# Kernel optimization log

Measured on AMD Instinct MI355X. Metric: run time of the kernel, lower is better.

Reference implementation:

```python
import jax, jax.numpy as jnp
import numpy as np

B, DIM, N = 4, 256, 2048
HEADS, DIM_HEAD = 8, 64
HIDDEN = HEADS * DIM_HEAD
SCALE = DIM_HEAD ** -0.5


def setup_inputs() -> dict:
    key = jax.random.key(0)
    k0, k1, k2, k3 = jax.random.split(key, 4)
    x = jax.random.normal(k0, (B, DIM, N), dtype=jnp.float32)
    # Conv1d kernel-size-1 weights == plain matrices over channels
    w_qkv = jax.random.normal(k1, (3 * HIDDEN, DIM), dtype=jnp.float32) * (DIM ** -0.5)
    w_out = jax.random.normal(k2, (DIM, HIDDEN), dtype=jnp.float32) * (HIDDEN ** -0.5)
    b_out = jax.random.normal(k3, (DIM,), dtype=jnp.float32) * 0.01
    return {"x": x, "w_qkv": w_qkv, "w_out": w_out, "b_out": b_out}


def reference(x, w_qkv, w_out, b_out):
    b, c, n = x.shape
    # 1x1 conv projection: [3H, C] x [b, C, n] -> [b, 3H, n]
    qkv = jnp.einsum('oc,bcn->bon', w_qkv, x)
    q, k, v = jnp.split(qkv, 3, axis=1)
    # [b, heads, dim_head, n]
    q = q.reshape(b, HEADS, DIM_HEAD, n) * SCALE
    k = k.reshape(b, HEADS, DIM_HEAD, n)
    v = v.reshape(b, HEADS, DIM_HEAD, n)
    sim = jnp.einsum('bhcn,bhcm->bhnm', q, k)          # [b,h,n,n]
    attn = jax.nn.softmax(sim, axis=-1)
    out = jnp.einsum('bhnm,bhcm->bhcn', attn, v)       # [b,h,dh,n]
    out = out.reshape(b, HIDDEN, n)
    return jnp.einsum('oc,bcn->bon', w_out, out) + b_out[None, :, None]
```

## Files before the change

### kernel.cpp

```cpp
#include <hip/hip_runtime.h>
#include <math.h>

#define BB 4
#define CDIM 256
#define NN 2048
#define HEADS 8
#define DH 64
#define HIDDEN 512
#define THREEH 1536
#define QSCALE 0.18033688011112042f

typedef __attribute__((ext_vector_type(8))) short bf16x8;
typedef __attribute__((ext_vector_type(4))) float f32x4;

static __device__ inline unsigned short f2bf(float f) {
    unsigned u = __float_as_uint(f);
    u += 0x7fff + ((u >> 16) & 1);
    return (unsigned short)(u >> 16);
}
#if __has_builtin(__builtin_amdgcn_cvt_pk_bf16_f32)
static __device__ inline unsigned pk2(float a, float b) {
    auto v = __builtin_amdgcn_cvt_pk_bf16_f32(a, b);
    return __builtin_bit_cast(unsigned, v);
}
#else
static __device__ inline unsigned pk2(float a, float b) {
    return (unsigned)f2bf(a) | ((unsigned)f2bf(b) << 16);
}
#endif
#if __has_builtin(__builtin_amdgcn_exp2f)
#define EXP2(x) __builtin_amdgcn_exp2f(x)
#else
#define EXP2(x) exp2f(x)
#endif
#define MFMA16(a, b, c) __builtin_amdgcn_mfma_f32_16x16x32_bf16(a, b, c, 0, 0, 0)
#define SWZC(row, ch) ((((ch) ^ ((row) & 7)) << 3))

__global__ __launch_bounds__(256) void prep_all(const float* __restrict__ x,
                                                const float* __restrict__ wqkv,
                                                const float* __restrict__ wout,
                                                unsigned short* __restrict__ Xt,
                                                unsigned* __restrict__ Wqb,
                                                unsigned* __restrict__ Wob) {
    __shared__ float Ls[64][65];
    const int bx = blockIdx.x;
    if (bx < 512) {
        const int n0 = (bx & 31) * 64, c0 = ((bx >> 5) & 3) * 64, b = bx >> 7;
        const int t = threadIdx.x;
        const int r16 = t >> 4, c16 = t & 15;
#pragma unroll
        for (int s = 0; s < 4; ++s) {
            const int c = s * 16 + r16;
            float4 v = *(const float4*)&x[((size_t)(b * CDIM + c0 + c)) * NN + n0 + c16 * 4];
            *(float4*)&Ls[c][c16 * 4] = v;
        }
        __syncthreads();
#pragma unroll
        for (int s = 0; s < 4; ++s) {
            const int n = s * 16 + r16;
            const int c4 = c16 * 4;
            uint2 u;
            u.x = pk2(Ls[c4][n], Ls[c4 + 1][n]);
            u.y = pk2(Ls[c4 + 2][n], Ls[c4 + 3][n]);
            *(uint2*)&Xt[((size_t)(b * NN) + n0 + n) * CDIM + c0 + c4] = u;
        }
    } else if (bx < 536) {
        const int tt = (bx - 512) * 256 + threadIdx.x;
#pragma unroll 4
        for (int j = 0; j < 16; ++j) {
            const int i4 = tt + j * 6144;
            const int e = i4 * 4;
            const float s = ((e >> 8) < HIDDEN) ? QSCALE : 1.f;
            float4 v = *(const float4*)&wqkv[e];
            Wqb[i4 * 2 + 0] = pk2(v.x * s, v.y * s);
            Wqb[i4 * 2 + 1] = pk2(v.z * s, v.w * s);
        }
    } else {
        const int tt = (bx - 536) * 256 + threadIdx.x;
#pragma unroll 4
        for (int j = 0; j < 16; ++j) {
            const int i4 = tt + j * 2048;
            const int e = i4 * 4;
            float4 v = *(const float4*)&wout[e];
            Wob[i4 * 2 + 0] = pk2(v.x, v.y);
            Wob[i4 * 2 + 1] = pk2(v.z, v.w);
        }
    }
}

__global__ __launch_bounds__(256, 3) void qkv_gemm(const unsigned short* __restrict__ Xt,
                                                   const unsigned short* __restrict__ Wqb,
                                                   unsigned short* __restrict__ Qb,
                                                   unsigned short* __restrict__ Kb,
                                                   unsigned short* __restrict__ Vb) {
    __shared__ unsigned short Xs[128 * 64], Ws[128 * 64];
    const int bn0 = blockIdx.x * 128, o0 = blockIdx.y * 128;
    const int t = threadIdx.x, l = t & 63, w = t >> 6, lo = l & 15, quad = l >> 4;
    const int wo = (w >> 1) * 64, wn = (w & 1) * 64;
    const int sr = t >> 1, scb = (t & 1) * 4;
    const bool isV = (o0 >= 2 * HIDDEN);
    f32x4 acc[4][4];
#pragma unroll
    for (int i = 0; i < 4; ++i)
#pragma unroll
        for (int j = 0; j < 4; ++j) acc[i][j] = (f32x4){0.f, 0.f, 0.f, 0.f};

    for (int kc = 0; kc < CDIM; kc += 64) {
        __syncthreads();
#pragma unroll
        for (int j = 0; j < 4; ++j) {
            const int ch = scb + j;
            *(uint4*)&Xs[sr * 64 + SWZC(sr, ch)] =
                *(const uint4*)&Xt[(size_t)(bn0 + sr) * CDIM + kc + ch * 8];
            *(uint4*)&Ws[sr * 64 + SWZC(sr, ch)] =
                *(const uint4*)&Wqb[(size_t)(o0 + sr) * CDIM + kc + ch * 8];
        }
        __syncthreads();
#pragma unroll
        for (int kk = 0; kk < 2; ++kk) {
            const int swz = SWZC(lo, kk * 4 + quad);
            if (!isV) {
                bf16x8 af[4], bv[4];
#pragma unroll
                for (int ot = 0; ot < 4; ++ot) af[ot] = *(const bf16x8*)&Ws[(wo + ot * 16 + lo) * 64 + swz];
#pragma unroll
                for (int nt = 0; nt < 4; ++nt) bv[nt] = *(const bf16x8*)&Xs[(wn + nt * 16 + lo) * 64 + swz];
#pragma unroll
                for (int ot = 0; ot < 4; ++ot)
#pragma unroll
                    for (int nt = 0; nt < 4; ++nt) acc[ot][nt] = MFMA16(af[ot], bv[nt], acc[ot][nt]);
            } else {
                bf16x8 af[4], bv[4];
#pragma unroll
                for (int mt = 0; mt < 4; ++mt) af[mt] = *(const bf16x8*)&Xs[(wn + mt * 16 + lo) * 64 + swz];
#pragma unroll
                for (int ot = 0; ot < 4; ++ot) bv[ot] = *(const bf16x8*)&Ws[(wo + ot * 16 + lo) * 64 + swz];
#pragma unroll
                for (int mt = 0; mt < 4; ++mt)
#pragma unroll
                    for (int ot = 0; ot < 4; ++ot) acc[mt][ot] = MFMA16(af[mt], bv[ot], acc[mt][ot]);
            }
        }
    }
    if (!isV) {
#pragma unroll
        for (int ot = 0; ot < 4; ++ot) {
            const int og = o0 + wo + ot * 16 + quad * 4;
            const int h = (og >> 6) & 7;
            const int c0 = og & 63;
            unsigned short* dst = (og >= HIDDEN) ? Kb : Qb;
#pragma unroll
            for (int nt = 0; nt < 4; ++nt) {
                const int bn = bn0 + wn + nt * 16 + lo;
                const int b = bn >> 11, n = bn & 2047;
                uint2 u;
                u.x = pk2(acc[ot][nt][0], acc[ot][nt][1]);
                u.y = pk2(acc[ot][nt][2], acc[ot][nt][3]);
                *(uint2*)&dst[(((size_t)(b * HEADS + h)) * NN + n) * DH + c0] = u;
            }
        }
    } else {
#pragma unroll
        for (int mt = 0; mt < 4; ++mt) {
            const int bn = bn0 + wn + mt * 16 + quad * 4;
            const int b = bn >> 11, m = bn & 2047;
#pragma unroll
            for (int ot = 0; ot < 4; ++ot) {
                const int og = o0 + wo + ot * 16 + lo;
                const int h = (og >> 6) & 7;
                const int c = og & 63;
                uint2 u;
                u.x = pk2(acc[mt][ot][0], acc[mt][ot][1]);
                u.y = pk2(acc[mt][ot][2], acc[mt][ot][3]);
                *(uint2*)&Vb[(((size_t)(b * HEADS + h)) * DH + c) * NN + m] = u;
            }
        }
    }
}

__global__ __launch_bounds__(256, 4) void flash_attn(const unsigned short* __restrict__ Qb,
                                                     const unsigned short* __restrict__ Kb,
                                                     const unsigned short* __restrict__ Vb,
                                                     unsigned short* __restrict__ Yb) {
    __shared__ unsigned short Ks[64 * 64], Vs[64 * 64], Ps[128 * 64];
    const int flat = blockIdx.x;
    const int rest = flat >> 3;
    const int bh = ((rest & 3) << 3) | (flat & 7);
    const int q0 = (rest >> 2) * 128;
    const int b = bh >> 3, h = bh & 7;
    const int t = threadIdx.x, l = t & 63, w = t >> 6, lo = l & 15, quad = l >> 4;
    const unsigned short* Qp = Qb + (size_t)bh * NN * DH;
    const unsigned short* Kp = Kb + (size_t)bh * NN * DH;
    const unsigned short* Vp = Vb + (size_t)bh * DH * NN;
    const int qbase = q0 + 32 * w;
    bf16x8 bQ[2][2];
#pragma unroll
    for (int qt = 0; qt < 2; ++qt)
#pragma unroll
        for (int hh = 0; hh < 2; ++hh)
            bQ[qt][hh] = *(const bf16x8*)&Qp[(size_t)(qbase + qt * 16 + lo) * DH + hh * 32 + quad * 8];
    f32x4 O[4][2], lacc[2];
#pragma unroll
    for (int i = 0; i < 4; ++i)
#pragma unroll
        for (int j = 0; j < 2; ++j) O[i][j] = (f32x4){0.f, 0.f, 0.f, 0.f};
#pragma unroll
    for (int j = 0; j < 2; ++j) lacc[j] = (f32x4){0.f, 0.f, 0.f, 0.f};
    const int sr = t >> 3, sc = t & 7;
    const int kst0 = sr * 64 + SWZC(sr, sc);
    const int key = lo & 7;
    bf16x8 aOnes;
    {
        const short v = (lo == 0) ? (short)0x3F80 : (short)0;
        aOnes = (bf16x8){v, v, v, v, v, v, v, v};
    }
    uint4 rk0 = *(const uint4*)&Kp[(size_t)sr * DH + sc * 8];
    uint4 rk1 = *(const uint4*)&Kp[(size_t)(sr + 32) * DH + sc * 8];
    uint4 rv0 = *(const uint4*)&Vp[(size_t)sr * NN + sc * 8];
    uint4 rv1 = *(const uint4*)&Vp[(size_t)(sr + 32) * NN + sc * 8];

#pragma unroll 1
    for (int m0 = 0; m0 < NN; m0 += 64) {
        __syncthreads();
        *(uint4*)&Ks[kst0] = rk0;
        *(uint4*)&Ks[kst0 + 2048] = rk1;
        *(uint4*)&Vs[kst0] = rv0;
        *(uint4*)&Vs[kst0 + 2048] = rv1;
        __syncthreads();
        {
            const int m1 = (m0 + 64 < NN) ? (m0 + 64) : m0;
            rk0 = *(const uint4*)&Kp[(size_t)(m1 + sr) * DH + sc * 8];
            rk1 = *(const uint4*)&Kp[(size_t)(m1 + sr + 32) * DH + sc * 8];
            rv0 = *(const uint4*)&Vp[(size_t)sr * NN + m1 + sc * 8];
            rv1 = *(const uint4*)&Vp[(size_t)(sr + 32) * NN + m1 + sc * 8];
        }
#pragma unroll
        for (int nt = 0; nt < 4; ++nt) {
            const int rb = (nt * 16 + lo) * 64;
            bf16x8 a0 = *(const bf16x8*)&Ks[rb + SWZC(lo, quad)];
            bf16x8 a1 = *(const bf16x8*)&Ks[rb + SWZC(lo, quad + 4)];
            const int pcol = (((nt * 2 + (quad >> 1)) ^ key) << 3) + (quad & 1) * 4;
#pragma unroll
            for (int qt = 0; qt < 2; ++qt) {
                f32x4 z = (f32x4){0.f, 0.f, 0.f, 0.f};
                z = MFMA16(a0, bQ[qt][0], z);
                z = MFMA16(a1, bQ[qt][1], z);
                f32x4 p;
#pragma unroll
                for (int i = 0; i < 4; ++i) p[i] = EXP2(z[i]);
                uint2 u;
                u.x = pk2(p[0], p[1]);
                u.y = pk2(p[2], p[3]);
                *(uint2*)&Ps[(32 * w + qt * 16 + lo) * 64 + pcol] = u;
            }
        }
        asm volatile("s_waitcnt lgkmcnt(0)" ::: "memory");
        bf16x8 pb[2][2];
#pragma unroll
        for (int qt = 0; qt < 2; ++qt) {
            const int prow = (32 * w + qt * 16 + lo) * 64;
            pb[qt][0] = *(const bf16x8*)&Ps[prow + SWZC(lo, quad)];
            pb[qt][1] = *(const bf16x8*)&Ps[prow + SWZC(lo, quad + 4)];
        }
#pragma unroll
        for (int ct = 0; ct < 4; ++ct) {
            const int rb = (ct * 16 + lo) * 64;
            bf16x8 a0 = *(const bf16x8*)&Vs[rb + SWZC(lo, quad)];
            bf16x8 a1 = *(const bf16x8*)&Vs[rb + SWZC(lo, quad + 4)];
#pragma unroll
            for (int qt = 0; qt < 2; ++qt) {
                O[ct][qt] = MFMA16(a0, pb[qt][0], O[ct][qt]);
                O[ct][qt] = MFMA16(a1, pb[qt][1], O[ct][qt]);
            }
        }
#pragma unroll
        for (int qt = 0; qt < 2; ++qt) {
            lacc[qt] = MFMA16(aOnes, pb[qt][0], lacc[qt]);
            lacc[qt] = MFMA16(aOnes, pb[qt][1], lacc[qt]);
        }
    }
#pragma unroll
    for (int qt = 0; qt < 2; ++qt) {
        const float lv = __shfl(lacc[qt][0], lo);
        const float inv = 1.f / lv;
        const int q = qbase + qt * 16 + lo;
        unsigned short* yrow = Yb + ((size_t)(b * NN) + q) * HIDDEN + h * DH;
#pragma unroll
        for (int ct = 0; ct < 4; ++ct) {
            uint2 u;
            u.x = pk2(O[ct][qt][0] * inv, O[ct][qt][1] * inv);
            u.y = pk2(O[ct][qt][2] * inv, O[ct][qt][3] * inv);
            *(uint2*)&yrow[ct * 16 + quad * 4] = u;
        }
    }
}

__global__ __launch_bounds__(256, 4) void out_gemm(const unsigned short* __restrict__ Yb,
                                                   const unsigned short* __restrict__ Wob,
                                                   const float* __restrict__ bias,
                                                   float* __restrict__ out) {
    __shared__ unsigned short Ys[128 * 64], Wos[64 * 64];
    const int bn0 = blockIdx.x * 128, o0 = blockIdx.y * 64;
    const int t = threadIdx.x, l = t & 63, w = t >> 6, lo = l & 15, quad = l >> 4;
    const int wn = w * 32;
    const int sr = t >> 1, scb = (t & 1) * 4;
    const int sr2 = t >> 2, scb2 = (t & 3) * 2;
    f32x4 acc[2][4];
#pragma unroll
    for (int i = 0; i < 2; ++i)
#pragma unroll
        for (int j = 0; j < 4; ++j) acc[i][j] = (f32x4){0.f, 0.f, 0.f, 0.f};

    for (int kc = 0; kc < HIDDEN; kc += 64) {
        __syncthreads();
#pragma unroll
        for (int j = 0; j < 4; ++j) {
            const int ch = scb + j;
            *(uint4*)&Ys[sr * 64 + SWZC(sr, ch)] =
                *(const uint4*)&Yb[(size_t)(bn0 + sr) * HIDDEN + kc + ch * 8];
        }
#pragma unroll
        for (int j = 0; j < 2; ++j) {
            const int ch = scb2 + j;
            *(uint4*)&Wos[sr2 * 64 + SWZC(sr2, ch)] =
                *(const uint4*)&Wob[(size_t)(o0 + sr2) * HIDDEN + kc + ch * 8];
        }
        __syncthreads();
#pragma unroll
        for (int kk = 0; kk < 2; ++kk) {
            const int swz = SWZC(lo, kk * 4 + quad);
            bf16x8 bv[4];
#pragma unroll
            for (int ot = 0; ot < 4; ++ot) bv[ot] = *(const bf16x8*)&Wos[(ot * 16 + lo) * 64 + swz];
#pragma unroll
            for (int mt = 0; mt < 2; ++mt) {
                bf16x8 av = *(const bf16x8*)&Ys[(wn + mt * 16 + lo) * 64 + swz];
#pragma unroll
                for (int ot = 0; ot < 4; ++ot) acc[mt][ot] = MFMA16(av, bv[ot], acc[mt][ot]);
            }
        }
    }
#pragma unroll
    for (int mt = 0; mt < 2; ++mt) {
        const int bn = bn0 + wn + mt * 16 + quad * 4;
        const int b = bn >> 11, n = bn & 2047;
#pragma unroll
        for (int ot = 0; ot < 4; ++ot) {
            const int o = o0 + ot * 16 + lo;
            *(f32x4*)&out[((size_t)(b * CDIM + o)) * NN + n] = acc[mt][ot] + bias[o];
        }
    }
}

extern "C" void kernel_launch(void* const* d_in, const int* in_sizes, int n_in,
                              void* d_out, int out_size, void* d_ws, size_t ws_size,
                              hipStream_t stream) {
    const float* x     = (const float*)d_in[0];
    const float* w_qkv = (const float*)d_in[1];
    const float* w_out = (const float*)d_in[2];
    const float* b_out = (const float*)d_in[3];
    float* out = (float*)d_out;

    unsigned short* Wqb = (unsigned short*)d_ws;
    unsigned short* Wob = Wqb + (size_t)THREEH * CDIM;
    unsigned short* Xt  = Wob + (size_t)CDIM * HIDDEN;
    unsigned short* Qb  = Xt + (size_t)BB * NN * CDIM;
    unsigned short* Kb  = Qb + (size_t)BB * HEADS * NN * DH;
    unsigned short* Vb  = Kb + (size_t)BB * HEADS * NN * DH;
    unsigned short* Yb  = Vb + (size_t)BB * HEADS * DH * NN;

    prep_all<<<544, 256, 0, stream>>>(x, w_qkv, w_out, Xt, (unsigned*)Wqb, (unsigned*)Wob);
    qkv_gemm<<<dim3(BB * NN / 128, THREEH / 128), 256, 0, stream>>>(Xt, Wqb, Qb, Kb, Vb);
    flash_attn<<<512, 256, 0, stream>>>(Qb, Kb, Vb, Yb);
    out_gemm<<<dim3(BB * NN / 128, CDIM / 64), 256, 0, stream>>>(Yb, Wob, b_out, out);
}
```

Before: 147.8 us.

## Prefetch GEMM tiles into registers and read K/V directly from global in attention

The QKV and output projection GEMMs now load the next K-chunk of their tiles into registers while the current chunk is being computed, a software-pipelined register prefetch. The flash attention kernel drops its shared-memory K/V staging and both barriers per iteration, and each wave reads its K and V MFMA fragments straight from global memory. This removes LDS traffic and block synchronization in attention, but every wave now fetches K/V separately with less coalesced 16-byte loads and relies on L1/L2 caching. There is also no explicit prefetch to hide the global load latency.

Result: slower. 256.6 us (+73.6%).

```diff
diff --git a/kernel.cpp b/kernel.cpp
--- a/kernel.cpp
+++ b/kernel.cpp
@@ -105,17 +105,30 @@
 #pragma unroll
         for (int j = 0; j < 4; ++j) acc[i][j] = (f32x4){0.f, 0.f, 0.f, 0.f};
 
+    uint4 rx[4], rw[4];
+#pragma unroll
+    for (int j = 0; j < 4; ++j) {
+        rx[j] = *(const uint4*)&Xt[(size_t)(bn0 + sr) * CDIM + (scb + j) * 8];
+        rw[j] = *(const uint4*)&Wqb[(size_t)(o0 + sr) * CDIM + (scb + j) * 8];
+    }
+#pragma unroll 1
     for (int kc = 0; kc < CDIM; kc += 64) {
         __syncthreads();
 #pragma unroll
         for (int j = 0; j < 4; ++j) {
             const int ch = scb + j;
-            *(uint4*)&Xs[sr * 64 + SWZC(sr, ch)] =
-                *(const uint4*)&Xt[(size_t)(bn0 + sr) * CDIM + kc + ch * 8];
-            *(uint4*)&Ws[sr * 64 + SWZC(sr, ch)] =
-                *(const uint4*)&Wqb[(size_t)(o0 + sr) * CDIM + kc + ch * 8];
-        }
-        __syncthreads();
+            *(uint4*)&Xs[sr * 64 + SWZC(sr, ch)] = rx[j];
+            *(uint4*)&Ws[sr * 64 + SWZC(sr, ch)] = rw[j];
+        }
+        __syncthreads();
+        {
+            const int kn = (kc + 64 < CDIM) ? kc + 64 : kc;
+#pragma unroll
+            for (int j = 0; j < 4; ++j) {
+                rx[j] = *(const uint4*)&Xt[(size_t)(bn0 + sr) * CDIM + kn + (scb + j) * 8];
+                rw[j] = *(const uint4*)&Wqb[(size_t)(o0 + sr) * CDIM + kn + (scb + j) * 8];
+            }
+        }
 #pragma unroll
         for (int kk = 0; kk < 2; ++kk) {
             const int swz = SWZC(lo, kk * 4 + quad);
@@ -182,7 +195,7 @@
                                                      const unsigned short* __restrict__ Kb,
                                                      const unsigned short* __restrict__ Vb,
                                                      unsigned short* __restrict__ Yb) {
-    __shared__ unsigned short Ks[64 * 64], Vs[64 * 64], Ps[128 * 64];
+    __shared__ unsigned short Ps[128 * 64];
     const int flat = blockIdx.x;
     const int rest = flat >> 3;
     const int bh = ((rest & 3) << 3) | (flat & 7);
@@ -206,39 +219,20 @@
         for (int j = 0; j < 2; ++j) O[i][j] = (f32x4){0.f, 0.f, 0.f, 0.f};
 #pragma unroll
     for (int j = 0; j < 2; ++j) lacc[j] = (f32x4){0.f, 0.f, 0.f, 0.f};
-    const int sr = t >> 3, sc = t & 7;
-    const int kst0 = sr * 64 + SWZC(sr, sc);
     const int key = lo & 7;
     bf16x8 aOnes;
     {
         const short v = (lo == 0) ? (short)0x3F80 : (short)0;
         aOnes = (bf16x8){v, v, v, v, v, v, v, v};
     }
-    uint4 rk0 = *(const uint4*)&Kp[(size_t)sr * DH + sc * 8];
-    uint4 rk1 = *(const uint4*)&Kp[(size_t)(sr + 32) * DH + sc * 8];
-    uint4 rv0 = *(const uint4*)&Vp[(size_t)sr * NN + sc * 8];
-    uint4 rv1 = *(const uint4*)&Vp[(size_t)(sr + 32) * NN + sc * 8];
 
 #pragma unroll 1
     for (int m0 = 0; m0 < NN; m0 += 64) {
-        __syncthreads();
-        *(uint4*)&Ks[kst0] = rk0;
-        *(uint4*)&Ks[kst0 + 2048] = rk1;
-        *(uint4*)&Vs[kst0] = rv0;
-        *(uint4*)&Vs[kst0 + 2048] = rv1;
-        __syncthreads();
-        {
-            const int m1 = (m0 + 64 < NN) ? (m0 + 64) : m0;
-            rk0 = *(const uint4*)&Kp[(size_t)(m1 + sr) * DH + sc * 8];
-            rk1 = *(const uint4*)&Kp[(size_t)(m1 + sr + 32) * DH + sc * 8];
-            rv0 = *(const uint4*)&Vp[(size_t)sr * NN + m1 + sc * 8];
-            rv1 = *(const uint4*)&Vp[(size_t)(sr + 32) * NN + m1 + sc * 8];
-        }
 #pragma unroll
         for (int nt = 0; nt < 4; ++nt) {
-            const int rb = (nt * 16 + lo) * 64;
-            bf16x8 a0 = *(const bf16x8*)&Ks[rb + SWZC(lo, quad)];
-            bf16x8 a1 = *(const bf16x8*)&Ks[rb + SWZC(lo, quad + 4)];
+            const unsigned short* kr = Kp + (size_t)(m0 + nt * 16 + lo) * DH + quad * 8;
+            bf16x8 a0 = *(const bf16x8*)kr;
+            bf16x8 a1 = *(const bf16x8*)(kr + 32);
             const int pcol = (((nt * 2 + (quad >> 1)) ^ key) << 3) + (quad & 1) * 4;
 #pragma unroll
             for (int qt = 0; qt < 2; ++qt) {
@@ -264,9 +258,9 @@
         }
 #pragma unroll
         for (int ct = 0; ct < 4; ++ct) {
-            const int rb = (ct * 16 + lo) * 64;
-            bf16x8 a0 = *(const bf16x8*)&Vs[rb + SWZC(lo, quad)];
-            bf16x8 a1 = *(const bf16x8*)&Vs[rb + SWZC(lo, quad + 4)];
+            const unsigned short* vr = Vp + (size_t)(ct * 16 + lo) * NN + m0 + quad * 8;
+            bf16x8 a0 = *(const bf16x8*)vr;
+            bf16x8 a1 = *(const bf16x8*)(vr + 32);
 #pragma unroll
             for (int qt = 0; qt < 2; ++qt) {
                 O[ct][qt] = MFMA16(a0, pb[qt][0], O[ct][qt]);
@@ -311,21 +305,31 @@
 #pragma unroll
         for (int j = 0; j < 4; ++j) acc[i][j] = (f32x4){0.f, 0.f, 0.f, 0.f};
 
+    uint4 ry[4], rw2[2];
+#pragma unroll
+    for (int j = 0; j < 4; ++j)
+        ry[j] = *(const uint4*)&Yb[(size_t)(bn0 + sr) * HIDDEN + (scb + j) * 8];
+#pragma unroll
+    for (int j = 0; j < 2; ++j)
+        rw2[j] = *(const uint4*)&Wob[(size_t)(o0 + sr2) * HIDDEN + (scb2 + j) * 8];
+
+#pragma unroll 1
     for (int kc = 0; kc < HIDDEN; kc += 64) {
         __syncthreads();
 #pragma unroll
-        for (int j = 0; j < 4; ++j) {
-            const int ch = scb + j;
-            *(uint4*)&Ys[sr * 64 + SWZC(sr, ch)] =
-                *(const uint4*)&Yb[(size_t)(bn0 + sr) * HIDDEN + kc + ch * 8];
-        }
-#pragma unroll
-        for (int j = 0; j < 2; ++j) {
-            const int ch = scb2 + j;
-            *(uint4*)&Wos[sr2 * 64 + SWZC(sr2, ch)] =
-                *(const uint4*)&Wob[(size_t)(o0 + sr2) * HIDDEN + kc + ch * 8];
-        }
-        __syncthreads();
+        for (int j = 0; j < 4; ++j) *(uint4*)&Ys[sr * 64 + SWZC(sr, scb + j)] = ry[j];
+#pragma unroll
+        for (int j = 0; j < 2; ++j) *(uint4*)&Wos[sr2 * 64 + SWZC(sr2, scb2 + j)] = rw2[j];
+        __syncthreads();
+        {
+            const int kn = (kc + 64 < HIDDEN) ? kc + 64 : kc;
+#pragma unroll
+            for (int j = 0; j < 4; ++j)
+                ry[j] = *(const uint4*)&Yb[(size_t)(bn0 + sr) * HIDDEN + kn + (scb + j) * 8];
+#pragma unroll
+            for (int j = 0; j < 2; ++j)
+                rw2[j] = *(const uint4*)&Wob[(size_t)(o0 + sr2) * HIDDEN + kn + (scb2 + j) * 8];
+        }
 #pragma unroll
         for (int kk = 0; kk < 2; ++kk) {
             const int swz = SWZC(lo, kk * 4 + quad);
```

## Stage GEMM and attention epilogues through LDS for coalesced 16-byte global stores

Applied to the files above, without the earlier changes.

The epilogues of qkv_gemm, flash_attn and out_gemm now write accumulator fragments into swizzled shared memory, synchronize, then read back contiguous rows so each thread issues full 16-byte vector stores to Q/K/V, Y and the fp32 output. Previously each lane wrote scattered 8-byte or strided chunks, which wasted memory transactions. The change costs extra LDS traffic and barriers, and it reuses the existing shared buffers as staging space.

Measured after the change: 156.5 us. +5.9%, slower.

```diff
diff --git a/kernel.cpp b/kernel.cpp
--- a/kernel.cpp
+++ b/kernel.cpp
@@ -93,7 +93,9 @@
                                                    unsigned short* __restrict__ Qb,
                                                    unsigned short* __restrict__ Kb,
                                                    unsigned short* __restrict__ Vb) {
-    __shared__ unsigned short Xs[128 * 64], Ws[128 * 64];
+    __shared__ unsigned short SB[16384];
+    unsigned short* Xs = SB;
+    unsigned short* Ws = SB + 8192;
     const int bn0 = blockIdx.x * 128, o0 = blockIdx.y * 128;
     const int t = threadIdx.x, l = t & 63, w = t >> 6, lo = l & 15, quad = l >> 4;
     const int wo = (w >> 1) * 64, wn = (w & 1) * 64;
@@ -142,39 +144,61 @@
             }
         }
     }
+    __syncthreads();
+    const int bb = bn0 >> 11, n_glob = bn0 & 2047;
     if (!isV) {
 #pragma unroll
         for (int ot = 0; ot < 4; ++ot) {
-            const int og = o0 + wo + ot * 16 + quad * 4;
-            const int h = (og >> 6) & 7;
-            const int c0 = og & 63;
-            unsigned short* dst = (og >= HIDDEN) ? Kb : Qb;
+            const int p = (wo >> 2) + ot * 4 + quad;
 #pragma unroll
             for (int nt = 0; nt < 4; ++nt) {
-                const int bn = bn0 + wn + nt * 16 + lo;
-                const int b = bn >> 11, n = bn & 2047;
+                const int nn = wn + nt * 16 + lo;
                 uint2 u;
                 u.x = pk2(acc[ot][nt][0], acc[ot][nt][1]);
                 u.y = pk2(acc[ot][nt][2], acc[ot][nt][3]);
-                *(uint2*)&dst[(((size_t)(b * HEADS + h)) * NN + n) * DH + c0] = u;
-            }
-        }
+                *(uint2*)&SB[nn * 128 + ((p ^ (nn & 31)) << 2)] = u;
+            }
+        }
+        __syncthreads();
+        const bool isK = (o0 >= HIDDEN);
+        const int hbase = (o0 - (isK ? HIDDEN : 0)) >> 6;
+        unsigned short* dst = isK ? Kb : Qb;
+        const int nn = t & 127, e = t >> 7;
+        uint2 gbuf[16];
+#pragma unroll
+        for (int j = 0; j < 16; ++j) {
+            const int p = e * 16 + j;
+            gbuf[j] = *(const uint2*)&SB[nn * 128 + ((p ^ (nn & 31)) << 2)];
+        }
+        unsigned short* drow = dst + (((size_t)(bb * HEADS + hbase + e)) * NN + n_glob + nn) * DH;
+#pragma unroll
+        for (int j = 0; j < 8; ++j) *(uint4*)&drow[j * 8] = *(uint4*)&gbuf[j * 2];
     } else {
 #pragma unroll
         for (int mt = 0; mt < 4; ++mt) {
-            const int bn = bn0 + wn + mt * 16 + quad * 4;
-            const int b = bn >> 11, m = bn & 2047;
+            const int p = (wn >> 2) + mt * 4 + quad;
 #pragma unroll
             for (int ot = 0; ot < 4; ++ot) {
-                const int og = o0 + wo + ot * 16 + lo;
-                const int h = (og >> 6) & 7;
-                const int c = og & 63;
+                const int oo = wo + ot * 16 + lo;
                 uint2 u;
                 u.x = pk2(acc[mt][ot][0], acc[mt][ot][1]);
                 u.y = pk2(acc[mt][ot][2], acc[mt][ot][3]);
-                *(uint2*)&Vb[(((size_t)(b * HEADS + h)) * DH + c) * NN + m] = u;
-            }
-        }
+                *(uint2*)&SB[oo * 128 + ((p ^ (oo & 31)) << 2)] = u;
+            }
+        }
+        __syncthreads();
+        const int hbase = (o0 - 2 * HIDDEN) >> 6;
+        const int oo = t >> 1, mh = t & 1;
+        uint2 gbuf[16];
+#pragma unroll
+        for (int j = 0; j < 16; ++j) {
+            const int p = mh * 16 + j;
+            gbuf[j] = *(const uint2*)&SB[oo * 128 + ((p ^ (oo & 31)) << 2)];
+        }
+        const int h = hbase + (oo >> 6), c = oo & 63;
+        unsigned short* drow = Vb + (((size_t)(bb * HEADS + h)) * DH + c) * NN + n_glob + mh * 64;
+#pragma unroll
+        for (int j = 0; j < 8; ++j) *(uint4*)&drow[j * 8] = *(uint4*)&gbuf[j * 2];
     }
 }
 
@@ -283,15 +307,28 @@
     for (int qt = 0; qt < 2; ++qt) {
         const float lv = __shfl(lacc[qt][0], lo);
         const float inv = 1.f / lv;
-        const int q = qbase + qt * 16 + lo;
-        unsigned short* yrow = Yb + ((size_t)(b * NN) + q) * HIDDEN + h * DH;
+        const int qr = 32 * w + qt * 16 + lo;
 #pragma unroll
         for (int ct = 0; ct < 4; ++ct) {
+            const int p = ct * 4 + quad;
             uint2 u;
             u.x = pk2(O[ct][qt][0] * inv, O[ct][qt][1] * inv);
             u.y = pk2(O[ct][qt][2] * inv, O[ct][qt][3] * inv);
-            *(uint2*)&yrow[ct * 16 + quad * 4] = u;
-        }
+            *(uint2*)&Ps[qr * 64 + ((p ^ (qr & 15)) << 2)] = u;
+        }
+    }
+    __syncthreads();
+    {
+        const int qr = t & 127, e = t >> 7;
+        uint2 gbuf[8];
+#pragma unroll
+        for (int j = 0; j < 8; ++j) {
+            const int p = e * 8 + j;
+            gbuf[j] = *(const uint2*)&Ps[qr * 64 + ((p ^ (qr & 15)) << 2)];
+        }
+        unsigned short* yrow = Yb + ((size_t)(b * NN) + q0 + qr) * HIDDEN + h * DH + e * 32;
+#pragma unroll
+        for (int j = 0; j < 4; ++j) *(uint4*)&yrow[j * 8] = *(uint4*)&gbuf[j * 2];
     }
 }
 
@@ -340,15 +377,33 @@
             }
         }
     }
-#pragma unroll
-    for (int mt = 0; mt < 2; ++mt) {
-        const int bn = bn0 + wn + mt * 16 + quad * 4;
-        const int b = bn >> 11, n = bn & 2047;
-#pragma unroll
-        for (int ot = 0; ot < 4; ++ot) {
-            const int o = o0 + ot * 16 + lo;
-            *(f32x4*)&out[((size_t)(b * CDIM + o)) * NN + n] = acc[mt][ot] + bias[o];
-        }
+    const int bb = bn0 >> 11, n_glob = bn0 & 2047;
+    float* LF = (float*)Ys;
+#pragma unroll
+    for (int pass = 0; pass < 2; ++pass) {
+        __syncthreads();
+#pragma unroll
+        for (int ot2 = 0; ot2 < 2; ++ot2) {
+            const int ot = pass * 2 + ot2;
+            const int oL = ot2 * 16 + lo;
+            const float bv = bias[o0 + ot * 16 + lo];
+#pragma unroll
+            for (int mt = 0; mt < 2; ++mt) {
+                const int g = (wn >> 2) + mt * 4 + quad;
+                *(f32x4*)&LF[oL * 128 + ((g ^ (oL & 31)) << 2)] = acc[mt][ot] + bv;
+            }
+        }
+        __syncthreads();
+        const int oL = t >> 3, seg = t & 7;
+        f32x4 fb[4];
+#pragma unroll
+        for (int j = 0; j < 4; ++j) {
+            const int g = seg * 4 + j;
+            fb[j] = *(const f32x4*)&LF[oL * 128 + ((g ^ (oL & 31)) << 2)];
+        }
+        float* orow = out + ((size_t)(bb * CDIM + o0 + pass * 32 + oL)) * NN + n_glob + seg * 16;
+#pragma unroll
+        for (int j = 0; j < 4; ++j) *(f32x4*)&orow[j * 4] = fb[j];
     }
 }
 
```
